# Kernel optimization log

Measured on AMD Instinct MI355X. Metric: run time of the kernel, lower is better.

The kernel has to match this reference:

```python
import jax, jax.numpy as jnp
import numpy as np

N_NODES = 100000
DEG = 16   # regular-graph degree -> every per-node subgraph is a (DEG+1)-node star
DIM = 128


def _crelu(z):
    return (jax.nn.relu(z.real) + 1j * jax.nn.relu(z.imag)).astype(jnp.complex64)


def _evolution_row(deg, tr, ti):
    # get_node_adjacency keeps only edges incident to the center node, so A_i is the
    # star graph K_{1,deg} with the center at index 0 -- identical for every node of a
    # deg-regular graph, so U is computed once.
    n = deg + 1
    A = jnp.zeros((n, n), jnp.complex64).at[0, 1:].set(1.0).at[1:, 0].set(1.0)
    t = (tr + 1j * ti).astype(jnp.complex64)
    G = jax.scipy.linalg.expm(-1j * A * t)
    # torch: sqrt(max eigval of G G^dagger); G G^dagger is Hermitian PSD -> eigvalsh
    s = jnp.sqrt(jnp.max(jnp.linalg.eigvalsh(G @ G.conj().T))).astype(jnp.complex64)
    Lt = G / s
    # np.sqrt on a matrix is ELEMENTWISE sqrt in the torch code -- replicate that
    Rt = jnp.sqrt(jnp.eye(n, dtype=jnp.complex64) - Lt @ (G.conj().T / s))
    # torch converts complex_time via .item() into numpy: no grad through U
    return jax.lax.stop_gradient(Lt[0] + Rt[0])  # (deg+1,) complex row 0 of [[Lt,Rt],[Rt,-Lt]]


def _layer(h, nbrs, Wr, Wi, br, bi, tr, ti, ebr, ebi):
    W = (Wr + 1j * Wi).astype(jnp.complex64)
    b = (br + 1j * bi).astype(jnp.complex64)
    h = _crelu(h @ W.T + b)
    deg = nbrs.shape[1]
    w = _evolution_row(deg, tr, ti)
    # evolved[0] = w[0]*h_i + sum_k w[1+k]*h_{sorted_nbr_k(i)}
    out = w[0] * h
    for k in range(deg):  # fixed small unrolled loop; avoids a [N, deg+1, C] intermediate
        out = out + w[1 + k] * h[nbrs[:, k]]
    return out + (ebr + 1j * ebi).astype(jnp.complex64)


def setup_inputs():
    key = jax.random.key(0)
    ks = jax.random.split(key, 12)
    x = jax.random.normal(ks[0], (N_NODES, DIM), jnp.float32)
    # circulant DEG-regular graph: node i ~ i +/- k (mod N), k=1..DEG/2; each undirected edge once
    K = DEG // 2
    i = np.arange(N_NODES)
    src = np.repeat(i, K)
    dst = ((i[:, None] + np.arange(1, K + 1)[None, :]) % N_NODES).reshape(-1)
    edge_index = jnp.asarray(np.stack([src, dst]), dtype=jnp.int32)
    sc = 0.05
    d = {"x": x, "edge_index": edge_index}
    for l, k0 in ((1, 1), (2, 6)):
        d[f"W{l}r"] = jax.random.normal(ks[k0], (DIM, DIM), jnp.float32) * sc
        d[f"W{l}i"] = jax.random.normal(ks[k0 + 1], (DIM, DIM), jnp.float32) * sc
        d[f"b{l}r"] = jax.random.normal(ks[k0 + 2], (DIM,), jnp.float32) * sc
        d[f"b{l}i"] = jax.random.normal(ks[k0 + 3], (DIM,), jnp.float32) * sc
        d[f"t{l}r"] = jnp.float32(1.0)
        d[f"t{l}i"] = jnp.float32(0.0)
        d[f"eb{l}r"] = jnp.zeros((DIM,), jnp.float32)
        d[f"eb{l}i"] = jnp.zeros((DIM,), jnp.float32)
    return d


def reference(x, edge_index, W1r, W1i, b1r, b1i, t1r, t1i, eb1r, eb1i,
              W2r, W2i, b2r, b2i, t2r, t2i, eb2r, eb2i):
    N = x.shape[0]
    src, dst = edge_index[0], edge_index[1]
    nodes = jnp.concatenate([src, dst])
    nbr = jnp.concatenate([dst, src])
    order = jnp.lexsort((nbr, nodes))        # sorted neighbor list per node
    deg = nodes.shape[0] // N                # regular graph -> static degree
    nbrs = nbr[order].reshape(N, deg)        # [N, DEG]
    h = x.astype(jnp.complex64)              # prepare_complex_input
    h = _layer(h, nbrs, W1r, W1i, b1r, b1i, t1r, t1i, eb1r, eb1i)
    h = _layer(h, nbrs, W2r, W2i, b2r, b2i, t2r, t2i, eb2r, eb2i)
    return h.real                            # output_type='real'
```

## Files before the change

kernel.cpp:

```cpp
#include <hip/hip_runtime.h>
#include <hip/hip_bf16.h>
#include <stdint.h>

typedef __attribute__((ext_vector_type(8))) short bf8_t;
typedef __attribute__((ext_vector_type(4))) float f32x4_t;
typedef __attribute__((ext_vector_type(4))) unsigned short us4_t;

#define MFMA_BF16 __builtin_amdgcn_mfma_f32_16x16x32_bf16

__device__ __forceinline__ unsigned short f2bf(float f) {
  union { float f; unsigned u; } x; x.f = f;
  unsigned r = (x.u + 0x7FFFu + ((x.u >> 16) & 1u)) >> 16;
  return (unsigned short)r;
}
__device__ __forceinline__ float bf2f(unsigned short b) {
  union { unsigned u; float f; } x; x.u = ((unsigned)b) << 16;
  return x.f;
}

__device__ __forceinline__ int xcd_swizzle(int b, int nwg) {
  const int NX = 8;
  int q = nwg / NX, r = nwg % NX;
  int xcd = b % NX, idx = b / NX;
  int start = (xcd < r) ? xcd * (q + 1) : r * (q + 1) + (xcd - r) * q;
  return start + idx;
}

__global__ void compute_wscal(const float* t1r, const float* t1i,
                              const float* t2r, const float* t2i,
                              float* wsc, int deg) {
  if (threadIdx.x != 0 || blockIdx.x != 0) return;
  float r = sqrtf((float)deg);
  for (int l = 0; l < 2; ++l) {
    float tr = l ? t2r[0] : t1r[0];
    float ti = l ? t2i[0] : t1i[0];
    float x = r * tr, y = r * ti;
    float cr = cosf(x) * coshf(y), ci = -sinf(x) * sinhf(y);
    float sr = sinf(x) * coshf(y), si = cosf(x) * sinhf(y);
    float a = cr * cr + ci * ci + sr * sr + si * si;
    float b = -2.0f * (ci * sr - cr * si);
    float s2 = fmaxf(a + fabsf(b), 1.0f);
    float s = sqrtf(s2);
    float l0r = cr / s, l0i = ci / s;
    float l1r = si / (r * s), l1i = -sr / (r * s);
    float q0 = 1.0f - a / s2;
    float r0r = (q0 >= 0.0f) ? sqrtf(q0) : 0.0f;
    float r0i = (q0 >= 0.0f) ? 0.0f : sqrtf(-q0);
    float q1 = -b / (r * s2);
    float r1r = (q1 >= 0.0f) ? sqrtf(q1) : 0.0f;
    float r1i = (q1 >= 0.0f) ? 0.0f : sqrtf(-q1);
    wsc[l * 4 + 0] = l0r + r0r;
    wsc[l * 4 + 1] = l0i + r0i;
    wsc[l * 4 + 2] = l1r + r1r;
    wsc[l * 4 + 3] = l1i + r1i;
  }
}

__device__ __forceinline__ void store_side(int* __restrict__ cnt,
                                           int* __restrict__ nbrs,
                                           int deg, int key, int val) {
  unsigned long long remaining = __ballot(1);
  unsigned long long mymask = 0;
  while (remaining) {
    int lead = __ffsll((long long)remaining) - 1;
    int lkey = __shfl(key, lead);
    unsigned long long m = __ballot(key == lkey);
    if (key == lkey) mymask = m;
    remaining &= ~m;
  }
  const int lane = threadIdx.x & 63;
  const int leader = __ffsll((long long)mymask) - 1;
  int base = 0;
  if (lane == leader) base = atomicAdd(&cnt[key], __popcll(mymask));
  base = __shfl(base, leader);
  const int rank = __popcll(mymask & ((1ull << lane) - 1ull));
  nbrs[(long)key * deg + base + rank] = val;
}

__global__ __launch_bounds__(256) void build_nbrs(
    const int* __restrict__ ei, int E, int* __restrict__ cnt,
    int* __restrict__ nbrs, int deg) {
  int e = blockIdx.x * 256 + threadIdx.x;
  if (e >= E) return;
  int s = ei[e], d = ei[E + e];
  store_side(cnt, nbrs, deg, s, d);
  store_side(cnt, nbrs, deg, d, s);
}

__device__ __forceinline__ void stage_w_plane(unsigned char* ldsW,
                                              const float* __restrict__ src,
                                              int tid) {
#pragma unroll
  for (int i = 0; i < 4; ++i) {
    const int e8 = (i * 512 + tid) * 8;
    float4 a = *(const float4*)(src + e8);
    float4 b = *(const float4*)(src + e8 + 4);
    union { bf8_t v; unsigned short s[8]; } o;
    o.s[0] = f2bf(a.x); o.s[1] = f2bf(a.y); o.s[2] = f2bf(a.z); o.s[3] = f2bf(a.w);
    o.s[4] = f2bf(b.x); o.s[5] = f2bf(b.y); o.s[6] = f2bf(b.z); o.s[7] = f2bf(b.w);
    const int c = e8 >> 7, k = e8 & 127;
    const int byte = c * 256 + ((k * 2) ^ ((c & 7) << 4));
    *(bf8_t*)(ldsW + byte) = o.v;
  }
}


__global__ __launch_bounds__(512, 4) void gemm_l1(
    const float* __restrict__ Xf,
    const float* __restrict__ Wr, const float* __restrict__ Wi,
    const float* __restrict__ br, const float* __restrict__ bi,
    unsigned short* __restrict__ H1, int n) {
  __shared__ unsigned char ldsW[32768];
  const int tid = threadIdx.x;
  const int wv = tid >> 6, lane = tid & 63;
  const int fr = lane & 15, kg = lane >> 4;
  const int lb = xcd_swizzle(blockIdx.x, gridDim.x);
  const int rowbase = lb * 128 + wv * 16;
  const int node = min(rowbase + fr, n - 1);
  const long a_off = (long)node * 128;

  stage_w_plane(ldsW, Wr, tid);

  bf8_t a[4];
#pragma unroll
  for (int ks = 0; ks < 4; ++ks) {
    const int koff = ks * 32 + kg * 8;
    float4 u = *(const float4*)(Xf + a_off + koff);
    float4 v = *(const float4*)(Xf + a_off + koff + 4);
    union { bf8_t vv; unsigned short s[8]; } t;
    t.s[0] = f2bf(u.x); t.s[1] = f2bf(u.y); t.s[2] = f2bf(u.z); t.s[3] = f2bf(u.w);
    t.s[4] = f2bf(v.x); t.s[5] = f2bf(v.y); t.s[6] = f2bf(v.z); t.s[7] = f2bf(v.w);
    a[ks] = t.vv;
  }
  __syncthreads();

  f32x4_t accr[8], acci[8];
#pragma unroll
  for (int i = 0; i < 8; ++i) { accr[i] = (f32x4_t)0.0f; acci[i] = (f32x4_t)0.0f; }

#pragma unroll
  for (int cf = 0; cf < 8; ++cf) {
    const int c = cf * 16 + fr;
    const int cbyte = c * 256, swz = (c & 7) << 4;
#pragma unroll
    for (int ks = 0; ks < 4; ++ks) {
      const int kb = (ks * 32 + kg * 8) * 2;
      bf8_t w = *(const bf8_t*)(ldsW + cbyte + (kb ^ swz));
      accr[cf] = MFMA_BF16(w, a[ks], accr[cf], 0, 0, 0);
    }
  }
  __syncthreads();
  stage_w_plane(ldsW, Wi, tid);
  __syncthreads();
#pragma unroll
  for (int cf = 0; cf < 8; ++cf) {
    const int c = cf * 16 + fr;
    const int cbyte = c * 256, swz = (c & 7) << 4;
#pragma unroll
    for (int ks = 0; ks < 4; ++ks) {
      const int kb = (ks * 32 + kg * 8) * 2;
      bf8_t w = *(const bf8_t*)(ldsW + cbyte + (kb ^ swz));
      acci[cf] = MFMA_BF16(w, a[ks], acci[cf], 0, 0, 0);
    }
  }

  const int onode = rowbase + fr;
  if (onode < n) {
    const long obase = (long)onode * 256;
#pragma unroll
    for (int cf = 0; cf < 8; ++cf) {
      const int cb = cf * 16 + kg * 4;
      const int chunk = cb >> 3, sub = cb & 7;
      union { float4 f4; float f[4]; } b4r, b4i;
      b4r.f4 = *(const float4*)(br + cb);
      b4i.f4 = *(const float4*)(bi + cb);
      us4_t pr, pi;
#pragma unroll
      for (int j = 0; j < 4; ++j) {
        pr[j] = f2bf(fmaxf(accr[cf][j] + b4r.f[j], 0.0f));
        pi[j] = f2bf(fmaxf(acci[cf][j] + b4i.f[j], 0.0f));
      }
      *(us4_t*)(H1 + obase + chunk * 16 + sub) = pr;
      *(us4_t*)(H1 + obase + chunk * 16 + 8 + sub) = pi;
    }
  }
}

template <int DEG>
__global__ __launch_bounds__(512, 4) void fused_l2(
    const unsigned short* __restrict__ H1,
    const int* __restrict__ nbrs, const float* __restrict__ wsc,
    const float* __restrict__ eb1r, const float* __restrict__ eb1i,
    const float* __restrict__ W2r, const float* __restrict__ W2i,
    const float* __restrict__ b2r, const float* __restrict__ b2i,
    unsigned short* __restrict__ H2, int n, int deg_rt) {
  __shared__ unsigned char ldsW[32768];
  __shared__ int ldsNB[128 * 17];
  const int tid = threadIdx.x;
  const int wv = tid >> 6, lane = tid & 63;
  const int fr = lane & 15, kg = lane >> 4;
  const int lb = xcd_swizzle(blockIdx.x, gridDim.x);
  const int rowbase = lb * 128 + wv * 16;
  const int node = min(rowbase + fr, n - 1);
  const int nloc = wv * 16 + fr;
  const float w0r = wsc[0], w0i = wsc[1], w1r = wsc[2], w1i = wsc[3];
  const int deg = DEG ? DEG : deg_rt;

  {
    const long base = (long)lb * 128 * deg;
    const long lim = (long)n * deg;
    for (int i = tid; i < 128 * deg; i += 512) {
      long gidx = base + i;
      int v = (gidx < lim) ? nbrs[gidx] : 0;
      v = min(max(v, 0), n - 1);
      ldsNB[(i / deg) * 17 + (i % deg)] = v;
    }
  }
  stage_w_plane(ldsW, W2r, tid);
  __syncthreads();

  bf8_t ar[4], ai[4];
#pragma unroll
  for (int ks = 0; ks < 4; ++ks) {
    const int ch16 = (ks * 4 + kg) * 16;
    union { bf8_t v; unsigned short s[8]; } o_r, o_i;
    o_r.v = *(const bf8_t*)(H1 + (long)node * 256 + ch16);
    o_i.v = *(const bf8_t*)(H1 + (long)node * 256 + ch16 + 8);
    float sr[8], si[8];
#pragma unroll
    for (int e = 0; e < 8; ++e) { sr[e] = 0.0f; si[e] = 0.0f; }
#pragma unroll
    for (int j = 0; j < (DEG ? DEG : 1); ++j) {
      for (int jj = DEG ? j : 0; jj < (DEG ? j + 1 : deg); ++jj) {
        const long m = (long)ldsNB[nloc * 17 + jj] * 256 + ch16;
        union { bf8_t v; unsigned short s[8]; } vr2, vi2;
        vr2.v = *(const bf8_t*)(H1 + m);
        vi2.v = *(const bf8_t*)(H1 + m + 8);
#pragma unroll
        for (int e = 0; e < 8; ++e) { sr[e] += bf2f(vr2.s[e]); si[e] += bf2f(vi2.s[e]); }
      }
    }
    const int koff = ks * 32 + kg * 8;
    union { float4 f4; float f[4]; } er0, er1, ei0, ei1;
    er0.f4 = *(const float4*)(eb1r + koff);
    er1.f4 = *(const float4*)(eb1r + koff + 4);
    ei0.f4 = *(const float4*)(eb1i + koff);
    ei1.f4 = *(const float4*)(eb1i + koff + 4);
    union { bf8_t v; unsigned short s[8]; } pr, pi;
#pragma unroll
    for (int e = 0; e < 8; ++e) {
      float hr = bf2f(o_r.s[e]), hi = bf2f(o_i.s[e]);
      float ebR = (e < 4) ? er0.f[e] : er1.f[e - 4];
      float ebI = (e < 4) ? ei0.f[e] : ei1.f[e - 4];
      float gr = w0r * hr - w0i * hi + w1r * sr[e] - w1i * si[e] + ebR;
      float gi = w0r * hi + w0i * hr + w1r * si[e] + w1i * sr[e] + ebI;
      pr.s[e] = f2bf(gr); pi.s[e] = f2bf(gi);
    }
    ar[ks] = pr.v; ai[ks] = pi.v;
  }

  f32x4_t accr[8], acci[8];
#pragma unroll
  for (int i = 0; i < 8; ++i) { accr[i] = (f32x4_t)0.0f; acci[i] = (f32x4_t)0.0f; }

#pragma unroll
  for (int cf = 0; cf < 8; ++cf) {
    const int c = cf * 16 + fr;
    const int cbyte = c * 256, swz = (c & 7) << 4;
#pragma unroll
    for (int ks = 0; ks < 4; ++ks) {
      const int kb = (ks * 32 + kg * 8) * 2;
      bf8_t w = *(const bf8_t*)(ldsW + cbyte + (kb ^ swz));
      accr[cf] = MFMA_BF16(w, ar[ks], accr[cf], 0, 0, 0);
      acci[cf] = MFMA_BF16(w, ai[ks], acci[cf], 0, 0, 0);
    }
  }
  __syncthreads();
  stage_w_plane(ldsW, W2i, tid);
  __syncthreads();

#pragma unroll
  for (int ks = 0; ks < 4; ++ks) {
    union { bf8_t v; unsigned u[4]; } t; t.v = ai[ks];
#pragma unroll
    for (int q = 0; q < 4; ++q) t.u[q] ^= 0x80008000u;
    ai[ks] = t.v;
  }
#pragma unroll
  for (int cf = 0; cf < 8; ++cf) {
    const int c = cf * 16 + fr;
    const int cbyte = c * 256, swz = (c & 7) << 4;
#pragma unroll
    for (int ks = 0; ks < 4; ++ks) {
      const int kb = (ks * 32 + kg * 8) * 2;
      bf8_t w = *(const bf8_t*)(ldsW + cbyte + (kb ^ swz));
      accr[cf] = MFMA_BF16(w, ai[ks], accr[cf], 0, 0, 0);
      acci[cf] = MFMA_BF16(w, ar[ks], acci[cf], 0, 0, 0);
    }
  }

  const int onode = rowbase + fr;
  if (onode < n) {
    const long obase = (long)onode * 256;
#pragma unroll
    for (int cf = 0; cf < 8; ++cf) {
      const int cb = cf * 16 + kg * 4;
      const int chunk = cb >> 3, sub = cb & 7;
      union { float4 f4; float f[4]; } b4r, b4i;
      b4r.f4 = *(const float4*)(b2r + cb);
      b4i.f4 = *(const float4*)(b2i + cb);
      us4_t pr, pi;
#pragma unroll
      for (int j = 0; j < 4; ++j) {
        pr[j] = f2bf(fmaxf(accr[cf][j] + b4r.f[j], 0.0f));
        pi[j] = f2bf(fmaxf(acci[cf][j] + b4i.f[j], 0.0f));
      }
      *(us4_t*)(H2 + obase + chunk * 16 + sub) = pr;
      *(us4_t*)(H2 + obase + chunk * 16 + 8 + sub) = pi;
    }
  }
}

template <int DEG>
__global__ __launch_bounds__(256) void agg_final(
    const unsigned short* __restrict__ H2,
    const int* __restrict__ nbrs, const float* __restrict__ wsc,
    const float* __restrict__ ebr,
    float* __restrict__ outf, int n, int deg_rt) {
  const int lb = xcd_swizzle(blockIdx.x, gridDim.x);
  const int g = lb * 256 + threadIdx.x;
  const int node = g >> 4;
  if (node >= n) return;
  const int g2 = g & 15;
  const int ch0 = g2 * 8;
  const int deg = DEG ? DEG : deg_rt;
  const float w0r = wsc[0], w0i = wsc[1], w1r = wsc[2], w1i = wsc[3];

  union { bf8_t v; unsigned short s[8]; } ur, ui;
  ur.v = *(const bf8_t*)(H2 + (long)node * 256 + g2 * 16);
  ui.v = *(const bf8_t*)(H2 + (long)node * 256 + g2 * 16 + 8);
  float srf[8], sif[8];
#pragma unroll
  for (int e = 0; e < 8; ++e) { srf[e] = 0.0f; sif[e] = 0.0f; }
  const int* nbp = nbrs + (long)node * deg;
#pragma unroll
  for (int k = 0; k < (DEG ? DEG : 1); ++k) {
    for (int kk = DEG ? k : 0; kk < (DEG ? k + 1 : deg); ++kk) {
      const long m = (long)nbp[kk] * 256 + g2 * 16;
      union { bf8_t v; unsigned short s[8]; } vr2, vi2;
      vr2.v = *(const bf8_t*)(H2 + m);
      vi2.v = *(const bf8_t*)(H2 + m + 8);
#pragma unroll
      for (int e = 0; e < 8; ++e) { srf[e] += bf2f(vr2.s[e]); sif[e] += bf2f(vi2.s[e]); }
    }
  }
  union { float4 f4; float f[4]; } o0, o1;
#pragma unroll
  for (int e = 0; e < 8; ++e) {
    const int c = ch0 + e;
    float hrf = bf2f(ur.s[e]), hif = bf2f(ui.s[e]);
    float R = w0r * hrf - w0i * hif + w1r * srf[e] - w1i * sif[e] + ebr[c];
    if (e < 4) o0.f[e] = R; else o1.f[e - 4] = R;
  }
  *(float4*)(outf + (long)node * 128 + ch0) = o0.f4;
  *(float4*)(outf + (long)node * 128 + ch0 + 4) = o1.f4;
}

extern "C" void kernel_launch(void* const* d_in, const int* in_sizes, int n_in,
                              void* d_out, int out_size, void* d_ws, size_t ws_size,
                              hipStream_t stream) {
  const float* x    = (const float*)d_in[0];
  const int*   ei   = (const int*)d_in[1];
  const float* W1r  = (const float*)d_in[2];
  const float* W1i  = (const float*)d_in[3];
  const float* b1r  = (const float*)d_in[4];
  const float* b1i  = (const float*)d_in[5];
  const float* t1r  = (const float*)d_in[6];
  const float* t1i  = (const float*)d_in[7];
  const float* eb1r = (const float*)d_in[8];
  const float* eb1i = (const float*)d_in[9];
  const float* W2r  = (const float*)d_in[10];
  const float* W2i  = (const float*)d_in[11];
  const float* b2r  = (const float*)d_in[12];
  const float* b2i  = (const float*)d_in[13];
  const float* t2r  = (const float*)d_in[14];
  const float* t2i  = (const float*)d_in[15];
  const float* eb2r = (const float*)d_in[16];
  const float* eb2i = (const float*)d_in[17];

  const int DIM = 128;
  const int N = in_sizes[0] / DIM;
  const int E = in_sizes[1] / 2;
  const int deg = (2 * E) / N;

  char* ws = (char*)d_ws;
  size_t off = 0;
  auto alloc = [&](size_t bytes) -> char* {
    char* p = ws + off;
    off += (bytes + 255) & ~(size_t)255;
    return p;
  };
  int* cnt  = (int*)alloc((size_t)N * 4);
  int* nbrs = (int*)alloc((size_t)N * deg * 4);
  float* wsc = (float*)alloc(8 * 4);
  const size_t nH = (size_t)N * DIM;
  unsigned short* h1 = (unsigned short*)alloc(nH * 4);
  unsigned short* h2 = (unsigned short*)alloc(nH * 4);
  (void)ws_size; (void)n_in; (void)out_size;

  hipMemsetAsync(cnt, 0, (size_t)N * 4, stream);
  build_nbrs<<<(E + 255) / 256, 256, 0, stream>>>(ei, E, cnt, nbrs, deg);
  compute_wscal<<<1, 64, 0, stream>>>(t1r, t1i, t2r, t2i, wsc, deg);

  const int gemm_blocks = (N + 127) / 128;
  const int agg_blocks = (N * 16 + 255) / 256;

  gemm_l1<<<gemm_blocks, 512, 0, stream>>>(x, W1r, W1i, b1r, b1i, h1, N);

  if (deg == 16) {
    fused_l2<16><<<gemm_blocks, 512, 0, stream>>>(h1, nbrs, wsc, eb1r, eb1i,
                                                  W2r, W2i, b2r, b2i, h2, N, deg);
    agg_final<16><<<agg_blocks, 256, 0, stream>>>(h2, nbrs, wsc + 4, eb2r,
                                                  (float*)d_out, N, deg);
  } else {
    fused_l2<0><<<gemm_blocks, 512, 0, stream>>>(h1, nbrs, wsc, eb1r, eb1i,
                                                 W2r, W2i, b2r, b2i, h2, N, deg);
    agg_final<0><<<agg_blocks, 256, 0, stream>>>(h2, nbrs, wsc + 4, eb2r,
                                                 (float*)d_out, N, deg);
  }
}
```

Measured before the change: 386.4 us.

## Stage contiguous neighbor window of features in LDS for locality-aware aggregation

Both aggregation kernels now load a contiguous window of node feature rows (block range plus a halo of 8 on each side) into swizzled LDS. They then gather neighbors from LDS whenever every neighbor index of the block falls inside that window, and fall back to global gathers otherwise. This replaces repeated scattered global/L2 gathers with one coalesced bulk load, relying on the circulant banded graph structure. In exchange it uses much more LDS and lowers fused_l2 occupancy (launch bounds 4 to 2 waves), and agg_final is reorganized to 512 threads covering 64 nodes.

```diff
diff --git a/kernel.cpp b/kernel.cpp
--- a/kernel.cpp
+++ b/kernel.cpp
@@ -186,8 +186,9 @@
   }
 }
 
+#define FWIN 144
 template <int DEG>
-__global__ __launch_bounds__(512, 4) void fused_l2(
+__global__ __launch_bounds__(512, 2) void fused_l2(
     const unsigned short* __restrict__ H1,
     const int* __restrict__ nbrs, const float* __restrict__ wsc,
     const float* __restrict__ eb1r, const float* __restrict__ eb1i,
@@ -195,44 +196,76 @@
     const float* __restrict__ b2r, const float* __restrict__ b2i,
     unsigned short* __restrict__ H2, int n, int deg_rt) {
   __shared__ unsigned char ldsW[32768];
+  __shared__ __align__(16) unsigned char ldsWin[FWIN * 512];
   __shared__ int ldsNB[128 * 17];
+  __shared__ int ldsFlag;
   const int tid = threadIdx.x;
   const int wv = tid >> 6, lane = tid & 63;
   const int fr = lane & 15, kg = lane >> 4;
   const int lb = xcd_swizzle(blockIdx.x, gridDim.x);
-  const int rowbase = lb * 128 + wv * 16;
+  const int blockstart = lb * 128;
+  const int rowbase = blockstart + wv * 16;
   const int node = min(rowbase + fr, n - 1);
   const int nloc = wv * 16 + fr;
+  const int winstart = blockstart - 8;
   const float w0r = wsc[0], w0i = wsc[1], w1r = wsc[2], w1i = wsc[3];
   const int deg = DEG ? DEG : deg_rt;
 
-  {
-    const long base = (long)lb * 128 * deg;
+  if (tid == 0) ldsFlag = (winstart >= 0 && winstart + FWIN <= n) ? 1 : 0;
+  __syncthreads();
+
+  if (DEG) {
+    const long base = (long)blockstart * deg;
     const long lim = (long)n * deg;
-    for (int i = tid; i < 128 * deg; i += 512) {
+    for (int i = tid; i < 128 * DEG; i += 512) {
       long gidx = base + i;
       int v = (gidx < lim) ? nbrs[gidx] : 0;
       v = min(max(v, 0), n - 1);
-      ldsNB[(i / deg) * 17 + (i % deg)] = v;
+      ldsNB[(i / DEG) * 17 + (i % DEG)] = v;
+      if ((unsigned)(v - winstart) >= (unsigned)FWIN) ldsFlag = 0;
+    }
+    for (int u = tid; u < FWIN * 32; u += 512) {
+      const int row = u >> 5, off16 = u & 31;
+      const int grow = min(max(winstart + row, 0), n - 1);
+      bf8_t v = *(const bf8_t*)(H1 + (long)grow * 256 + off16 * 8);
+      *(bf8_t*)(ldsWin + row * 512 + ((off16 * 16) ^ ((row & 7) << 4))) = v;
     }
   }
   stage_w_plane(ldsW, W2r, tid);
   __syncthreads();
+  const bool fast = DEG && ldsFlag;
 
   bf8_t ar[4], ai[4];
 #pragma unroll
   for (int ks = 0; ks < 4; ++ks) {
-    const int ch16 = (ks * 4 + kg) * 16;
+    const int ch32 = (ks * 4 + kg) * 32;
     union { bf8_t v; unsigned short s[8]; } o_r, o_i;
-    o_r.v = *(const bf8_t*)(H1 + (long)node * 256 + ch16);
-    o_i.v = *(const bf8_t*)(H1 + (long)node * 256 + ch16 + 8);
     float sr[8], si[8];
 #pragma unroll
     for (int e = 0; e < 8; ++e) { sr[e] = 0.0f; si[e] = 0.0f; }
-#pragma unroll
-    for (int j = 0; j < (DEG ? DEG : 1); ++j) {
-      for (int jj = DEG ? j : 0; jj < (DEG ? j + 1 : deg); ++jj) {
-        const long m = (long)ldsNB[nloc * 17 + jj] * 256 + ch16;
+    if (fast) {
+      const int s0 = nloc + 8, sw0 = (s0 & 7) << 4;
+      o_r.v = *(const bf8_t*)(ldsWin + s0 * 512 + (ch32 ^ sw0));
+      o_i.v = *(const bf8_t*)(ldsWin + s0 * 512 + ((ch32 | 16) ^ sw0));
+#pragma unroll
+      for (int j = 0; j < (DEG ? DEG : 1); ++j) {
+        const int slot = ldsNB[nloc * 17 + j] - winstart;
+        const unsigned char* p = ldsWin + slot * 512;
+        const int sw = (slot & 7) << 4;
+        union { bf8_t v; unsigned short s[8]; } vr2, vi2;
+        vr2.v = *(const bf8_t*)(p + (ch32 ^ sw));
+        vi2.v = *(const bf8_t*)(p + ((ch32 | 16) ^ sw));
+#pragma unroll
+        for (int e = 0; e < 8; ++e) { sr[e] += bf2f(vr2.s[e]); si[e] += bf2f(vi2.s[e]); }
+      }
+    } else {
+      const int ch16 = ch32 >> 1;
+      o_r.v = *(const bf8_t*)(H1 + (long)node * 256 + ch16);
+      o_i.v = *(const bf8_t*)(H1 + (long)node * 256 + ch16 + 8);
+      const int* nbp = nbrs + (long)node * deg;
+      for (int j = 0; j < deg; ++j) {
+        const int v = DEG ? ldsNB[nloc * 17 + j] : min(max(nbp[j], 0), n - 1);
+        const long m = (long)v * 256 + ch16;
         union { bf8_t v; unsigned short s[8]; } vr2, vi2;
         vr2.v = *(const bf8_t*)(H1 + m);
         vi2.v = *(const bf8_t*)(H1 + m + 8);
@@ -321,49 +354,100 @@
   }
 }
 
+#define AWIN 80
 template <int DEG>
-__global__ __launch_bounds__(256) void agg_final(
+__global__ __launch_bounds__(512, 4) void agg_final(
     const unsigned short* __restrict__ H2,
     const int* __restrict__ nbrs, const float* __restrict__ wsc,
     const float* __restrict__ ebr,
     float* __restrict__ outf, int n, int deg_rt) {
+  __shared__ __align__(16) unsigned char ldsWin[AWIN * 512];
+  __shared__ int ldsNB[64 * 17];
+  __shared__ int ldsFlag;
+  const int tid = threadIdx.x;
   const int lb = xcd_swizzle(blockIdx.x, gridDim.x);
-  const int g = lb * 256 + threadIdx.x;
-  const int node = g >> 4;
-  if (node >= n) return;
-  const int g2 = g & 15;
-  const int ch0 = g2 * 8;
+  const int blockstart = lb * 64;
+  const int winstart = blockstart - 8;
   const int deg = DEG ? DEG : deg_rt;
   const float w0r = wsc[0], w0i = wsc[1], w1r = wsc[2], w1i = wsc[3];
 
-  union { bf8_t v; unsigned short s[8]; } ur, ui;
-  ur.v = *(const bf8_t*)(H2 + (long)node * 256 + g2 * 16);
-  ui.v = *(const bf8_t*)(H2 + (long)node * 256 + g2 * 16 + 8);
-  float srf[8], sif[8];
-#pragma unroll
-  for (int e = 0; e < 8; ++e) { srf[e] = 0.0f; sif[e] = 0.0f; }
-  const int* nbp = nbrs + (long)node * deg;
-#pragma unroll
-  for (int k = 0; k < (DEG ? DEG : 1); ++k) {
-    for (int kk = DEG ? k : 0; kk < (DEG ? k + 1 : deg); ++kk) {
-      const long m = (long)nbp[kk] * 256 + g2 * 16;
-      union { bf8_t v; unsigned short s[8]; } vr2, vi2;
-      vr2.v = *(const bf8_t*)(H2 + m);
-      vi2.v = *(const bf8_t*)(H2 + m + 8);
-#pragma unroll
-      for (int e = 0; e < 8; ++e) { srf[e] += bf2f(vr2.s[e]); sif[e] += bf2f(vi2.s[e]); }
-    }
-  }
-  union { float4 f4; float f[4]; } o0, o1;
-#pragma unroll
-  for (int e = 0; e < 8; ++e) {
-    const int c = ch0 + e;
-    float hrf = bf2f(ur.s[e]), hif = bf2f(ui.s[e]);
-    float R = w0r * hrf - w0i * hif + w1r * srf[e] - w1i * sif[e] + ebr[c];
-    if (e < 4) o0.f[e] = R; else o1.f[e - 4] = R;
-  }
-  *(float4*)(outf + (long)node * 128 + ch0) = o0.f4;
-  *(float4*)(outf + (long)node * 128 + ch0 + 4) = o1.f4;
+  if (tid == 0) ldsFlag = (winstart >= 0 && winstart + AWIN <= n) ? 1 : 0;
+  __syncthreads();
+  if (DEG) {
+    const long base = (long)blockstart * deg;
+    const long lim = (long)n * deg;
+    for (int i = tid; i < 64 * DEG; i += 512) {
+      long gidx = base + i;
+      int v = (gidx < lim) ? nbrs[gidx] : 0;
+      v = min(max(v, 0), n - 1);
+      ldsNB[(i / DEG) * 17 + (i % DEG)] = v;
+      if ((unsigned)(v - winstart) >= (unsigned)AWIN) ldsFlag = 0;
+    }
+    for (int u = tid; u < AWIN * 32; u += 512) {
+      const int row = u >> 5, off16 = u & 31;
+      const int grow = min(max(winstart + row, 0), n - 1);
+      bf8_t v = *(const bf8_t*)(H2 + (long)grow * 256 + off16 * 8);
+      *(bf8_t*)(ldsWin + row * 512 + ((off16 * 16) ^ ((row & 7) << 4))) = v;
+    }
+  }
+  __syncthreads();
+  const bool fast = DEG && ldsFlag;
+
+#pragma unroll
+  for (int q = 0; q < 2; ++q) {
+    const int item = q * 512 + tid;
+    const int nloc = item >> 4, g2 = item & 15;
+    const int node = blockstart + nloc;
+    const int rnode = min(node, n - 1);
+    const int ch32 = g2 * 32;
+    union { bf8_t v; unsigned short s[8]; } ur, ui;
+    float srf[8], sif[8];
+#pragma unroll
+    for (int e = 0; e < 8; ++e) { srf[e] = 0.0f; sif[e] = 0.0f; }
+    if (fast) {
+      const int s0 = nloc + 8, sw0 = (s0 & 7) << 4;
+      ur.v = *(const bf8_t*)(ldsWin + s0 * 512 + (ch32 ^ sw0));
+      ui.v = *(const bf8_t*)(ldsWin + s0 * 512 + ((ch32 | 16) ^ sw0));
+#pragma unroll
+      for (int k = 0; k < (DEG ? DEG : 1); ++k) {
+        const int slot = ldsNB[nloc * 17 + k] - winstart;
+        const unsigned char* p = ldsWin + slot * 512;
+        const int sw = (slot & 7) << 4;
+        union { bf8_t v; unsigned short s[8]; } vr2, vi2;
+        vr2.v = *(const bf8_t*)(p + (ch32 ^ sw));
+        vi2.v = *(const bf8_t*)(p + ((ch32 | 16) ^ sw));
+#pragma unroll
+        for (int e = 0; e < 8; ++e) { srf[e] += bf2f(vr2.s[e]); sif[e] += bf2f(vi2.s[e]); }
+      }
+    } else {
+      const int ch16 = g2 * 16;
+      ur.v = *(const bf8_t*)(H2 + (long)rnode * 256 + ch16);
+      ui.v = *(const bf8_t*)(H2 + (long)rnode * 256 + ch16 + 8);
+      const int* nbp = nbrs + (long)rnode * deg;
+      for (int k = 0; k < deg; ++k) {
+        const int v = DEG ? ldsNB[nloc * 17 + k] : min(max(nbp[k], 0), n - 1);
+        const long m = (long)v * 256 + ch16;
+        union { bf8_t v; unsigned short s[8]; } vr2, vi2;
+        vr2.v = *(const bf8_t*)(H2 + m);
+        vi2.v = *(const bf8_t*)(H2 + m + 8);
+#pragma unroll
+        for (int e = 0; e < 8; ++e) { srf[e] += bf2f(vr2.s[e]); sif[e] += bf2f(vi2.s[e]); }
+      }
+    }
+    if (node < n) {
+      const int ch0 = g2 * 8;
+      union { float4 f4; float f[4]; } o0, o1;
+#pragma unroll
+      for (int e = 0; e < 8; ++e) {
+        const int c = ch0 + e;
+        float hrf = bf2f(ur.s[e]), hif = bf2f(ui.s[e]);
+        float R = w0r * hrf - w0i * hif + w1r * srf[e] - w1i * sif[e] + ebr[c];
+        if (e < 4) o0.f[e] = R; else o1.f[e - 4] = R;
+      }
+      *(float4*)(outf + (long)node * 128 + ch0) = o0.f4;
+      *(float4*)(outf + (long)node * 128 + ch0 + 4) = o1.f4;
+    }
+  }
 }
 
 extern "C" void kernel_launch(void* const* d_in, const int* in_sizes, int n_in,
@@ -413,19 +497,19 @@
   compute_wscal<<<1, 64, 0, stream>>>(t1r, t1i, t2r, t2i, wsc, deg);
 
   const int gemm_blocks = (N + 127) / 128;
-  const int agg_blocks = (N * 16 + 255) / 256;
+  const int agg_blocks = (N + 63) / 64;
 
   gemm_l1<<<gemm_blocks, 512, 0, stream>>>(x, W1r, W1i, b1r, b1i, h1, N);
 
   if (deg == 16) {
     fused_l2<16><<<gemm_blocks, 512, 0, stream>>>(h1, nbrs, wsc, eb1r, eb1i,
                                                   W2r, W2i, b2r, b2i, h2, N, deg);
-    agg_final<16><<<agg_blocks, 256, 0, stream>>>(h2, nbrs, wsc + 4, eb2r,
+    agg_final<16><<<agg_blocks, 512, 0, stream>>>(h2, nbrs, wsc + 4, eb2r,
                                                   (float*)d_out, N, deg);
   } else {
     fused_l2<0><<<gemm_blocks, 512, 0, stream>>>(h1, nbrs, wsc, eb1r, eb1i,
                                                  W2r, W2i, b2r, b2i, h2, N, deg);
-    agg_final<0><<<agg_blocks, 256, 0, stream>>>(h2, nbrs, wsc + 4, eb2r,
+    agg_final<0><<<agg_blocks, 512, 0, stream>>>(h2, nbrs, wsc + 4, eb2r,
                                                  (float*)d_out, N, deg);
   }
 }
```

Result: faster. 323.1 us (-16.4%).
